# Performance work log

Measured on AMD Instinct MI355X. Metric: run time of the kernel, lower is better.

The kernel has to match this reference:

```python
import jax, jax.numpy as jnp
import numpy as np
import math

N_HEADS = 16
D_EFF = 64
ROPE_BASE = 500.0


def _rope(x, cos, sin):
    # x: (b, h, L, d_eff); cos/sin: (L, d_eff//2)
    x_even = x[..., 0::2]
    x_odd = x[..., 1::2]
    rot = jnp.stack([x_even * cos - x_odd * sin,
                     x_even * sin + x_odd * cos], axis=-1)
    return rot.reshape(x.shape)


def setup_inputs() -> dict:
    key = jax.random.key(0)
    ks = jax.random.split(key, 5)
    B, L, D = 1, 2048, 1024
    X = jax.random.normal(ks[0], (B, L, D), dtype=jnp.float32)
    # causal mask (1 = keep, 0 = masked), broadcastable to (B, h, L, L)
    mask = jnp.tril(jnp.ones((L, L), dtype=jnp.int32))[None, :, :]
    s = 1.0 / math.sqrt(D)
    Wq = jax.random.normal(ks[1], (D, D), dtype=jnp.float32) * s
    Wk = jax.random.normal(ks[2], (D, D), dtype=jnp.float32) * s
    Wv = jax.random.normal(ks[3], (D, D), dtype=jnp.float32) * s
    Wo = jax.random.normal(ks[4], (D, D), dtype=jnp.float32) * s
    return {"X": X, "mask": mask, "Wq": Wq, "Wk": Wk, "Wv": Wv, "Wo": Wo}


def reference(X, mask, Wq, Wk, Wv, Wo):
    b, L, d_model = X.shape
    h, d = N_HEADS, D_EFF
    d_full = h * d

    def split_heads(Y):
        return Y.reshape(b, L, h, d).transpose(0, 2, 1, 3)  # (b,h,L,d)

    Q = split_heads(X @ Wq)
    K = split_heads(X @ Wk)
    V = split_heads(X @ Wv)

    # interleaved RoPE, base 500
    inv_freq = 1.0 / (ROPE_BASE ** (jnp.arange(0, d, 2, dtype=jnp.float32) / d))
    freqs = jnp.arange(L, dtype=jnp.float32)[:, None] * inv_freq  # (L, d/2)
    cos, sin = jnp.cos(freqs), jnp.sin(freqs)
    Q = _rope(Q, cos, sin)
    K = _rope(K, cos, sin)

    S = jnp.einsum('bhqd,bhkd->bhqk', Q, K) / math.sqrt(d)
    S = jnp.where(mask[:, None, :, :] == 0, jnp.float32(-1e9), S)
    # NOTE: faithful to original torch code: softmax over the HEADS axis (dim=1)
    A = jax.nn.softmax(S, axis=1)
    Y = jnp.einsum('bhqk,bhkd->bhqd', A, V)
    Y = Y.transpose(0, 2, 1, 3).reshape(b, L, d_full)
    Y = Y @ Wo
    return Y * math.sqrt(d_model / d_full)
```

## Files before the change

kernel.cpp:

```cpp
#include <hip/hip_runtime.h>
#include <stdint.h>
#include <stddef.h>
#include <math.h>

typedef __attribute__((ext_vector_type(8))) short bf16x8;
typedef __attribute__((ext_vector_type(4))) short short4v;
typedef __attribute__((ext_vector_type(4))) float f32x4;

__device__ __forceinline__ short f2bf(float f) {
  union { float f; uint32_t u; } x; x.f = f;
  return (short)((x.u + 0x7fffu + ((x.u >> 16) & 1u)) >> 16);
}
__device__ __forceinline__ float bf2f(short s) {
  union { uint32_t u; float f; } x; x.u = ((uint32_t)(uint16_t)s) << 16;
  return x.f;
}
__device__ __forceinline__ uint32_t cvt_pk_bf16(float a, float b) {
  uint32_t r;
  asm("v_cvt_pk_bf16_f32 %0, %1, %2" : "=v"(r) : "v"(a), "v"(b));
  return r;
}

__device__ __forceinline__ void gload_lds16(const void* g, void* lds) {
  __builtin_amdgcn_global_load_lds(
      (const __attribute__((address_space(1))) void*)g,
      (__attribute__((address_space(3))) void*)lds, 16, 0, 0);
}

__global__ __launch_bounds__(256) void cast_b(const float* __restrict__ s,
                                              short* __restrict__ d) {
  int i4 = (blockIdx.x * 256 + threadIdx.x) * 4;
  float4 v = *(const float4*)&s[i4];
  short4v r = { f2bf(v.x), f2bf(v.y), f2bf(v.z), f2bf(v.w) };
  *(short4v*)&d[i4] = r;
}

__global__ __launch_bounds__(256) void reduce_y(const short* __restrict__ Ypc,
                                                const float* __restrict__ Cvs,
                                                short* __restrict__ o) {
  int q = blockIdx.x;
  int j = q >> 5, qr = q & 31;
  int a = j >> 2, r = j & 3;
  int base = (a + 1) * (2 * a + r);
  int nch = a + 1;
  int col = threadIdx.x * 4;
  float a0 = Cvs[col + 0], a1 = Cvs[col + 1], a2 = Cvs[col + 2], a3 = Cvs[col + 3];
  const short* p = Ypc + ((size_t)base * 32 + qr) * 1024 + col;
  for (int ch = 0; ch < nch; ch++) {
    short4v v = *(const short4v*)p;
    a0 += bf2f(v[0]); a1 += bf2f(v[1]); a2 += bf2f(v[2]); a3 += bf2f(v[3]);
    p += 32 * 1024;
  }
  uint32_t u0 = cvt_pk_bf16(a0, a1), u1 = cvt_pk_bf16(a2, a3);
  short4v rr = { (short)u0, (short)(u0 >> 16), (short)u1, (short)(u1 >> 16) };
  *(short4v*)&o[(size_t)q * 1024 + col] = rr;
}

__global__ __launch_bounds__(256) void transW(const float* __restrict__ Wq,
                                              const float* __restrict__ Wk,
                                              const float* __restrict__ Wv,
                                              const float* __restrict__ Wo,
                                              short* __restrict__ WcatT,
                                              short* __restrict__ WoT) {
  int z = blockIdx.z;
  const float* src = (z == 0) ? Wq : (z == 1) ? Wk : (z == 2) ? Wv : Wo;
  short* dst = (z == 3) ? WoT : WcatT + (size_t)z * 1024 * 1024;
  __shared__ float tl[32][33];
  int tx = threadIdx.x & 31, ty = threadIdx.x >> 5;
  int kk0 = blockIdx.x * 32;
  int nn0 = blockIdx.y * 32;
#pragma unroll
  for (int j = 0; j < 4; j++)
    tl[ty + j * 8][tx] = src[(size_t)(kk0 + ty + j * 8) * 1024 + nn0 + tx];
  __syncthreads();
#pragma unroll
  for (int j = 0; j < 4; j++)
    dst[(size_t)(nn0 + ty + j * 8) * 1024 + kk0 + tx] = f2bf(tl[tx][ty + j * 8]);
}

__global__ __launch_bounds__(256) void transpose_v(const short* __restrict__ Vb,
                                                   short* __restrict__ Vt) {
  __shared__ short tv[64][72];
  int h = blockIdx.y, k0 = blockIdx.x * 64;
  int tid = threadIdx.x;
#pragma unroll
  for (int j = 0; j < 2; j++) {
    int idx = tid + j * 256;
    int row = idx >> 3, c = idx & 7;
    bf16x8 v = *(const bf16x8*)&Vb[((size_t)h * 2048 + k0 + row) * 64 + c * 8];
#pragma unroll
    for (int t = 0; t < 8; t++) tv[row][c * 8 + t] = v[t];
  }
  __syncthreads();
#pragma unroll
  for (int j = 0; j < 2; j++) {
    int idx = tid + j * 256;
    int d = idx >> 3, c = idx & 7;
    bf16x8 v;
#pragma unroll
    for (int t = 0; t < 8; t++) v[t] = tv[c * 8 + t][d];
    *(bf16x8*)&Vt[((size_t)h * 64 + d) * 2048 + k0 + c * 8] = v;
  }
}

__global__ __launch_bounds__(256) void vsum(const short* __restrict__ Vb,
                                            float* __restrict__ Cvs) {
  __shared__ float red[16][17];
  int h = blockIdx.x >> 2, dq = blockIdx.x & 3;
  int dl = threadIdx.x & 15, ks = threadIdx.x >> 4;
  int d = dq * 16 + dl;
  float acc = 0.f;
  const short* base = &Vb[((size_t)h * 2048 + ks * 128) * 64 + d];
#pragma unroll 8
  for (int k = 0; k < 128; k++) acc += bf2f(base[(size_t)k * 64]);
  red[dl][ks] = acc;
  __syncthreads();
  if (threadIdx.x < 16) {
    float sum = 0.f;
#pragma unroll
    for (int i = 0; i < 16; i++) sum += red[threadIdx.x][i];
    Cvs[h * 64 + dq * 16 + threadIdx.x] = sum * 0.0625f;
  }
}

template <int MODE>
__global__ __launch_bounds__(256, 2)
void gemm_kernel(const short* __restrict__ A, const short* __restrict__ B,
                 int N, int K, float* __restrict__ C,
                 short* __restrict__ Qb, short* __restrict__ Kb,
                 short* __restrict__ Vb) {
  __shared__ __attribute__((aligned(16))) short lga[128 * 64];
  __shared__ __attribute__((aligned(16))) short lgb[128 * 64];
  const int tid = threadIdx.x;
  const int lane = tid & 63;
  const int w = tid >> 6;
  const int l15 = lane & 15;
  const int quad = lane >> 4;
  const int wm = w >> 1, wn = w & 1;
  const int m0 = blockIdx.x * 128, n0 = blockIdx.y * 128;
  const int rsub = lane >> 3;
  const int cpos = lane & 7;

  f32x4 acc[4][4];
#pragma unroll
  for (int i = 0; i < 4; i++)
#pragma unroll
    for (int j = 0; j < 4; j++) acc[i][j] = (f32x4){0.f, 0.f, 0.f, 0.f};

  for (int kb = 0; kb < K; kb += 64) {
    __syncthreads();
#pragma unroll
    for (int j = 0; j < 4; j++) {
      int r = (w * 4 + j) * 8 + rsub;
      int kc = cpos ^ rsub;
      gload_lds16(A + (size_t)(m0 + r) * K + kb + kc * 8, &lga[(w * 4 + j) * 512]);
      gload_lds16(B + (size_t)(n0 + r) * K + kb + kc * 8, &lgb[(w * 4 + j) * 512]);
    }
    __syncthreads();
#pragma unroll
    for (int kk = 0; kk < 2; kk++) {
      bf16x8 af[4], bfr[4];
#pragma unroll
      for (int t = 0; t < 4; t++) {
        int row = wm * 64 + t * 16 + l15;
        int pc = (kk * 4 + quad) ^ (row & 7);
        af[t] = *(const bf16x8*)&lga[row * 64 + pc * 8];
        int rowb = wn * 64 + t * 16 + l15;
        int pcb = (kk * 4 + quad) ^ (rowb & 7);
        bfr[t] = *(const bf16x8*)&lgb[rowb * 64 + pcb * 8];
      }
#pragma unroll
      for (int mt = 0; mt < 4; mt++)
#pragma unroll
        for (int nt = 0; nt < 4; nt++)
          acc[mt][nt] = __builtin_amdgcn_mfma_f32_16x16x32_bf16(
              af[mt], bfr[nt], acc[mt][nt], 0, 0, 0);
    }
  }

  if (MODE == 0) {
#pragma unroll
    for (int mt = 0; mt < 4; mt++) {
      int q = m0 + wm * 64 + mt * 16 + quad * 4;
#pragma unroll
      for (int nt = 0; nt < 4; nt++) {
        int n = n0 + wn * 64 + nt * 16 + l15;
#pragma unroll
        for (int r = 0; r < 4; r++) C[(size_t)(q + r) * N + n] = acc[mt][nt][r];
      }
    }
  } else {
#pragma unroll
    for (int mt = 0; mt < 4; mt++) {
#pragma unroll
      for (int nt = 0; nt < 4; nt++) {
        int n = n0 + wn * 64 + nt * 16 + l15;
        int mat = n >> 10;
        int h = (n >> 6) & 15;
        int d = n & 63;
#pragma unroll
        for (int r = 0; r < 4; r++) {
          int q = m0 + wm * 64 + mt * 16 + quad * 4 + r;
          float v = acc[mt][nt][r];
          float o = __shfl_xor(v, 1, 64);
          if (mat < 2) {
            int i = d >> 1;
            float ang = (float)q * __builtin_exp2f(-(float)i * 0.2801807588956902f);
            float sn, cs;
            __sincosf(ang, &sn, &cs);
            float rv = (d & 1) ? (o * sn + v * cs) : (v * cs - o * sn);
            short* dst = (mat == 0) ? Qb : Kb;
            dst[((size_t)h * 2048 + q) * 64 + d] = f2bf(rv);
          } else {
            Vb[((size_t)h * 2048 + q) * 64 + d] = f2bf(v);
          }
        }
      }
    }
  }
}

__global__ __launch_bounds__(1024, 2)
void attn_kernel(const short* __restrict__ Qb, const short* __restrict__ Kb,
                 const short* __restrict__ Vt, short* __restrict__ Ypc) {
  __shared__ short Sb[16 * 32 * 72];
  const int tid = threadIdx.x;
  const int lane = tid & 63;
  const int h = tid >> 6;
  const int l15 = lane & 15, quad = lane >> 4;
  const int b = blockIdx.x;
  int a = (int)((sqrtf((float)(2 * b + 1)) - 1.f) * 0.5f);
  while (2 * (a + 1) * (a + 2) <= b) a++;
  while (2 * a * (a + 1) > b) a--;
  const int off = b - 2 * a * (a + 1);
  const int den = a + 1;
  const int r = off / den;
  const int c = off - r * den;
  const int j = 4 * a + r;
  const int q0 = j * 32;
  const int G = (j + 2) >> 1;
  const int g0 = 2 * c;
  const int ng = (g0 + 2 <= G) ? 2 : 1;

  bf16x8 qf[2][2];
#pragma unroll
  for (int qs = 0; qs < 2; qs++)
#pragma unroll
    for (int cc = 0; cc < 2; cc++)
      qf[qs][cc] = *(const bf16x8*)&Qb[((size_t)h * 2048 + q0 + qs * 16 + l15) * 64 +
                                       cc * 32 + quad * 8];

  f32x4 yacc[2][4];
#pragma unroll
  for (int i = 0; i < 2; i++)
#pragma unroll
    for (int jj = 0; jj < 4; jj++) yacc[i][jj] = (f32x4){0.f, 0.f, 0.f, 0.f};

  for (int gi = 0; gi < ng; gi++) {
    const int k0 = (g0 + gi) * 64;
#pragma unroll
    for (int st = 0; st < 4; st++) {
      const short* kb = &Kb[((size_t)h * 2048 + k0 + st * 16 + l15) * 64 + quad * 8];
      bf16x8 kf0 = *(const bf16x8*)kb;
      bf16x8 kf1 = *(const bf16x8*)(kb + 32);
#pragma unroll
      for (int qs = 0; qs < 2; qs++) {
        f32x4 sa = (f32x4){0.f, 0.f, 0.f, 0.f};
        sa = __builtin_amdgcn_mfma_f32_16x16x32_bf16(qf[qs][0], kf0, sa, 0, 0, 0);
        sa = __builtin_amdgcn_mfma_f32_16x16x32_bf16(qf[qs][1], kf1, sa, 0, 0, 0);
        const float cs = 0.18033688011112042f;
        uint32_t u0 = cvt_pk_bf16(sa[0] * cs, sa[1] * cs);
        uint32_t u1 = cvt_pk_bf16(sa[2] * cs, sa[3] * cs);
        int rb = (h * 32 + qs * 16 + quad * 4) * 72 + st * 16 + l15;
        Sb[rb]       = (short)u0;
        Sb[rb + 72]  = (short)(u0 >> 16);
        Sb[rb + 144] = (short)u1;
        Sb[rb + 216] = (short)(u1 >> 16);
      }
    }
    __syncthreads();
#pragma unroll
    for (int pp = 0; pp < 2; pp++) {
      int p = tid + pp * 1024;
      int q = p >> 6, kl = p & 63;
      int base = q * 72 + kl;
      float t[16];
      float m = -1e30f;
#pragma unroll
      for (int hh = 0; hh < 16; hh++) {
        t[hh] = bf2f(Sb[hh * 2304 + base]);
        m = fmaxf(m, t[hh]);
      }
      float sum = 0.f;
#pragma unroll
      for (int hh = 0; hh < 16; hh++) {
        float e = __builtin_exp2f(t[hh] - m);
        t[hh] = e;
        sum += e;
      }
      bool msk = (k0 + kl) > (q0 + q);
      float rs = msk ? 0.f : 1.f / sum;
      float offv = msk ? 0.f : 0.0625f;
#pragma unroll
      for (int hh = 0; hh < 16; hh += 2) {
        uint32_t u = cvt_pk_bf16(t[hh] * rs - offv, t[hh + 1] * rs - offv);
        Sb[hh * 2304 + base]       = (short)u;
        Sb[(hh + 1) * 2304 + base] = (short)(u >> 16);
      }
    }
    __syncthreads();
#pragma unroll
    for (int kk = 0; kk < 2; kk++) {
      bf16x8 af0 = *(const bf16x8*)&Sb[(h * 32 + l15) * 72 + kk * 32 + quad * 8];
      bf16x8 af1 = *(const bf16x8*)&Sb[(h * 32 + 16 + l15) * 72 + kk * 32 + quad * 8];
#pragma unroll
      for (int nt = 0; nt < 4; nt++) {
        bf16x8 vf = *(const bf16x8*)&Vt[((size_t)h * 64 + nt * 16 + l15) * 2048 +
                                        k0 + kk * 32 + quad * 8];
        yacc[0][nt] = __builtin_amdgcn_mfma_f32_16x16x32_bf16(af0, vf, yacc[0][nt],
                                                              0, 0, 0);
        yacc[1][nt] = __builtin_amdgcn_mfma_f32_16x16x32_bf16(af1, vf, yacc[1][nt],
                                                              0, 0, 0);
      }
    }
    __syncthreads();
  }
  short* Y = Ypc + (size_t)b * 32 * 1024;
#pragma unroll
  for (int qs = 0; qs < 2; qs++) {
#pragma unroll
    for (int nt = 0; nt < 4; nt++) {
      int col = h * 64 + nt * 16 + l15;
#pragma unroll
      for (int rr = 0; rr < 4; rr++)
        Y[(size_t)(qs * 16 + quad * 4 + rr) * 1024 + col] = f2bf(yacc[qs][nt][rr]);
    }
  }
}

extern "C" void kernel_launch(void* const* d_in, const int* in_sizes, int n_in,
                              void* d_out, int out_size, void* d_ws, size_t ws_size,
                              hipStream_t stream) {
  (void)in_sizes; (void)n_in; (void)out_size; (void)ws_size;
  const float* X  = (const float*)d_in[0];
  const float* Wq = (const float*)d_in[2];
  const float* Wk = (const float*)d_in[3];
  const float* Wv = (const float*)d_in[4];
  const float* Wo = (const float*)d_in[5];
  char* ws = (char*)d_ws;
  const size_t MB = 1024 * 1024;
  short* Xbf   = (short*)(ws + 0);
  short* WcatT = (short*)(ws + 4 * MB);
  short* WoT   = (short*)(ws + 10 * MB);
  short* Qb    = (short*)(ws + 12 * MB);
  short* Kb    = (short*)(ws + 16 * MB);
  short* Vb    = (short*)(ws + 20 * MB);
  short* Vt    = (short*)(ws + 24 * MB);
  short* Ypc   = (short*)(ws + 28 * MB);
  float* Cvs   = (float*)(ws + 63 * MB);
  short* Ycbf  = Xbf;
  float* out   = (float*)d_out;

  cast_b<<<dim3(2048), dim3(256), 0, stream>>>(X, Xbf);
  transW<<<dim3(32, 32, 4), dim3(256), 0, stream>>>(Wq, Wk, Wv, Wo, WcatT, WoT);
  gemm_kernel<1><<<dim3(16, 24), dim3(256), 0, stream>>>(Xbf, WcatT, 3072, 1024,
                                                         nullptr, Qb, Kb, Vb);
  transpose_v<<<dim3(32, 16), dim3(256), 0, stream>>>(Vb, Vt);
  vsum<<<dim3(64), dim3(256), 0, stream>>>(Vb, Cvs);
  attn_kernel<<<dim3(544), dim3(1024), 0, stream>>>(Qb, Kb, Vt, Ypc);
  reduce_y<<<dim3(2048), dim3(256), 0, stream>>>(Ypc, Cvs, Ycbf);
  gemm_kernel<0><<<dim3(16, 8), dim3(256), 0, stream>>>(Ycbf, WoT, 1024, 1024,
                                                        out, nullptr, nullptr, nullptr);
}
```

Before: 223.0 us.

## Double attention query tile to 64 rows with new balanced block-to-chunk mapping

```diff
diff --git a/kernel.cpp b/kernel.cpp
--- a/kernel.cpp
+++ b/kernel.cpp
@@ -39,17 +39,23 @@
                                                 const float* __restrict__ Cvs,
                                                 short* __restrict__ o) {
   int q = blockIdx.x;
-  int j = q >> 5, qr = q & 31;
-  int a = j >> 2, r = j & 3;
-  int base = (a + 1) * (2 * a + r);
-  int nch = a + 1;
+  int j = q >> 6, qr = q & 63;
   int col = threadIdx.x * 4;
   float a0 = Cvs[col + 0], a1 = Cvs[col + 1], a2 = Cvs[col + 2], a3 = Cvs[col + 3];
-  const short* p = Ypc + ((size_t)base * 32 + qr) * 1024 + col;
-  for (int ch = 0; ch < nch; ch++) {
+  int cmax = j >> 1;
+  for (int c = 0; c <= cmax; c++) {
+    int slot;
+    if (j == 2 * c) {
+      slot = 256 + c;
+    } else if (c <= 7) {
+      slot = c + 8 * (j - 2 * c - 1);
+    } else {
+      int x = 15 - c;
+      slot = x + 8 * ((31 - 2 * x) + (j - 2 * c - 1));
+    }
+    const short* p = Ypc + ((size_t)slot * 64 + qr) * 1024 + col;
     short4v v = *(const short4v*)p;
     a0 += bf2f(v[0]); a1 += bf2f(v[1]); a2 += bf2f(v[2]); a3 += bf2f(v[3]);
-    p += 32 * 1024;
   }
   uint32_t u0 = cvt_pk_bf16(a0, a1), u1 = cvt_pk_bf16(a2, a3);
   short4v rr = { (short)u0, (short)(u0 >> 16), (short)u1, (short)(u1 >> 16) };
@@ -220,39 +226,39 @@
   }
 }
 
-__global__ __launch_bounds__(1024, 2)
+__global__ __launch_bounds__(1024, 1)
 void attn_kernel(const short* __restrict__ Qb, const short* __restrict__ Kb,
                  const short* __restrict__ Vt, short* __restrict__ Ypc) {
-  __shared__ short Sb[16 * 32 * 72];
+  __shared__ short Sb[16 * 64 * 72];
   const int tid = threadIdx.x;
   const int lane = tid & 63;
   const int h = tid >> 6;
   const int l15 = lane & 15, quad = lane >> 4;
   const int b = blockIdx.x;
-  int a = (int)((sqrtf((float)(2 * b + 1)) - 1.f) * 0.5f);
-  while (2 * (a + 1) * (a + 2) <= b) a++;
-  while (2 * a * (a + 1) > b) a--;
-  const int off = b - 2 * a * (a + 1);
-  const int den = a + 1;
-  const int r = off / den;
-  const int c = off - r * den;
-  const int j = 4 * a + r;
-  const int q0 = j * 32;
-  const int G = (j + 2) >> 1;
+  int c, j, ng;
+  if (b < 256) {
+    int x = b & 7, s = b >> 3;
+    int n1 = 31 - 2 * x;
+    if (s < n1) { c = x;      j = 2 * x + 1 + s; }
+    else        { c = 15 - x; j = 31 - 2 * x + (s - n1); }
+    ng = 2;
+  } else {
+    c = b - 256; j = 2 * c; ng = 1;
+  }
+  const int q0 = j * 64;
   const int g0 = 2 * c;
-  const int ng = (g0 + 2 <= G) ? 2 : 1;
-
-  bf16x8 qf[2][2];
-#pragma unroll
-  for (int qs = 0; qs < 2; qs++)
+
+  bf16x8 qf[4][2];
+#pragma unroll
+  for (int qs = 0; qs < 4; qs++)
 #pragma unroll
     for (int cc = 0; cc < 2; cc++)
       qf[qs][cc] = *(const bf16x8*)&Qb[((size_t)h * 2048 + q0 + qs * 16 + l15) * 64 +
                                        cc * 32 + quad * 8];
 
-  f32x4 yacc[2][4];
-#pragma unroll
-  for (int i = 0; i < 2; i++)
+  f32x4 yacc[4][4];
+#pragma unroll
+  for (int i = 0; i < 4; i++)
 #pragma unroll
     for (int jj = 0; jj < 4; jj++) yacc[i][jj] = (f32x4){0.f, 0.f, 0.f, 0.f};
 
@@ -264,14 +270,14 @@
       bf16x8 kf0 = *(const bf16x8*)kb;
       bf16x8 kf1 = *(const bf16x8*)(kb + 32);
 #pragma unroll
-      for (int qs = 0; qs < 2; qs++) {
+      for (int qs = 0; qs < 4; qs++) {
         f32x4 sa = (f32x4){0.f, 0.f, 0.f, 0.f};
         sa = __builtin_amdgcn_mfma_f32_16x16x32_bf16(qf[qs][0], kf0, sa, 0, 0, 0);
         sa = __builtin_amdgcn_mfma_f32_16x16x32_bf16(qf[qs][1], kf1, sa, 0, 0, 0);
         const float cs = 0.18033688011112042f;
         uint32_t u0 = cvt_pk_bf16(sa[0] * cs, sa[1] * cs);
         uint32_t u1 = cvt_pk_bf16(sa[2] * cs, sa[3] * cs);
-        int rb = (h * 32 + qs * 16 + quad * 4) * 72 + st * 16 + l15;
+        int rb = (h * 64 + qs * 16 + quad * 4) * 72 + st * 16 + l15;
         Sb[rb]       = (short)u0;
         Sb[rb + 72]  = (short)(u0 >> 16);
         Sb[rb + 144] = (short)u1;
@@ -279,8 +285,8 @@
       }
     }
     __syncthreads();
-#pragma unroll
-    for (int pp = 0; pp < 2; pp++) {
+#pragma unroll 1
+    for (int pp = 0; pp < 4; pp++) {
       int p = tid + pp * 1024;
       int q = p >> 6, kl = p & 63;
       int base = q * 72 + kl;
@@ -288,7 +294,7 @@
       float m = -1e30f;
 #pragma unroll
       for (int hh = 0; hh < 16; hh++) {
-        t[hh] = bf2f(Sb[hh * 2304 + base]);
+        t[hh] = bf2f(Sb[hh * 4608 + base]);
         m = fmaxf(m, t[hh]);
       }
       float sum = 0.f;
@@ -304,30 +310,32 @@
 #pragma unroll
       for (int hh = 0; hh < 16; hh += 2) {
         uint32_t u = cvt_pk_bf16(t[hh] * rs - offv, t[hh + 1] * rs - offv);
-        Sb[hh * 2304 + base]       = (short)u;
-        Sb[(hh + 1) * 2304 + base] = (short)(u >> 16);
+        Sb[hh * 4608 + base]       = (short)u;
+        Sb[(hh + 1) * 4608 + base] = (short)(u >> 16);
       }
     }
     __syncthreads();
 #pragma unroll
     for (int kk = 0; kk < 2; kk++) {
-      bf16x8 af0 = *(const bf16x8*)&Sb[(h * 32 + l15) * 72 + kk * 32 + quad * 8];
-      bf16x8 af1 = *(const bf16x8*)&Sb[(h * 32 + 16 + l15) * 72 + kk * 32 + quad * 8];
+      bf16x8 af[4];
+#pragma unroll
+      for (int qs = 0; qs < 4; qs++)
+        af[qs] = *(const bf16x8*)&Sb[(h * 64 + qs * 16 + l15) * 72 + kk * 32 + quad * 8];
 #pragma unroll
       for (int nt = 0; nt < 4; nt++) {
         bf16x8 vf = *(const bf16x8*)&Vt[((size_t)h * 64 + nt * 16 + l15) * 2048 +
                                         k0 + kk * 32 + quad * 8];
-        yacc[0][nt] = __builtin_amdgcn_mfma_f32_16x16x32_bf16(af0, vf, yacc[0][nt],
-                                                              0, 0, 0);
-        yacc[1][nt] = __builtin_amdgcn_mfma_f32_16x16x32_bf16(af1, vf, yacc[1][nt],
-                                                              0, 0, 0);
-      }
-    }
-    __syncthreads();
-  }
-  short* Y = Ypc + (size_t)b * 32 * 1024;
-#pragma unroll
-  for (int qs = 0; qs < 2; qs++) {
+#pragma unroll
+        for (int qs = 0; qs < 4; qs++)
+          yacc[qs][nt] = __builtin_amdgcn_mfma_f32_16x16x32_bf16(af[qs], vf,
+                                                                 yacc[qs][nt], 0, 0, 0);
+      }
+    }
+    __syncthreads();
+  }
+  short* Y = Ypc + (size_t)b * 64 * 1024;
+#pragma unroll
+  for (int qs = 0; qs < 4; qs++) {
 #pragma unroll
     for (int nt = 0; nt < 4; nt++) {
       int col = h * 64 + nt * 16 + l15;
@@ -367,7 +375,7 @@
                                                          nullptr, Qb, Kb, Vb);
   transpose_v<<<dim3(32, 16), dim3(256), 0, stream>>>(Vb, Vt);
   vsum<<<dim3(64), dim3(256), 0, stream>>>(Vb, Cvs);
-  attn_kernel<<<dim3(544), dim3(1024), 0, stream>>>(Qb, Kb, Vt, Ypc);
+  attn_kernel<<<dim3(272), dim3(1024), 0, stream>>>(Qb, Kb, Vt, Ypc);
   reduce_y<<<dim3(2048), dim3(256), 0, stream>>>(Ypc, Cvs, Ycbf);
   gemm_kernel<0><<<dim3(16, 8), dim3(256), 0, stream>>>(Ycbf, WoT, 1024, 1024,
                                                         out, nullptr, nullptr, nullptr);
```

Result: slower. 232.3 us (+4.2%).

## Remap attention block schedule to balanced slots and drop softmax max pass

Applied to the files above, without the earlier changes.

```diff
diff --git a/kernel.cpp b/kernel.cpp
--- a/kernel.cpp
+++ b/kernel.cpp
@@ -40,16 +40,22 @@
                                                 short* __restrict__ o) {
   int q = blockIdx.x;
   int j = q >> 5, qr = q & 31;
-  int a = j >> 2, r = j & 3;
-  int base = (a + 1) * (2 * a + r);
-  int nch = a + 1;
   int col = threadIdx.x * 4;
   float a0 = Cvs[col + 0], a1 = Cvs[col + 1], a2 = Cvs[col + 2], a3 = Cvs[col + 3];
-  const short* p = Ypc + ((size_t)base * 32 + qr) * 1024 + col;
-  for (int ch = 0; ch < nch; ch++) {
+  int cf = (j - 2) >> 2;
+  for (int c = 0; c <= cf; c++) {
+    int slot = (c <= 7) ? (c + 8 * (j - 4 * c - 2)) : ((15 - c) + 8 * j);
+    const short* p = Ypc + ((size_t)slot * 32 + qr) * 1024 + col;
     short4v v = *(const short4v*)p;
     a0 += bf2f(v[0]); a1 += bf2f(v[1]); a2 += bf2f(v[2]); a3 += bf2f(v[3]);
-    p += 32 * 1024;
+  }
+  if ((j & 3) < 2) {
+    int cp = j >> 2;
+    int slot = (cp <= 7) ? (cp + 8 * (64 + (j & 3)))
+                         : ((15 - cp) + 8 * (66 + (j & 3)));
+    const short* p = Ypc + ((size_t)slot * 32 + qr) * 1024 + col;
+    short4v v = *(const short4v*)p;
+    a0 += bf2f(v[0]); a1 += bf2f(v[1]); a2 += bf2f(v[2]); a3 += bf2f(v[3]);
   }
   uint32_t u0 = cvt_pk_bf16(a0, a1), u1 = cvt_pk_bf16(a2, a3);
   short4v rr = { (short)u0, (short)(u0 >> 16), (short)u1, (short)(u1 >> 16) };
@@ -229,18 +235,15 @@
   const int h = tid >> 6;
   const int l15 = lane & 15, quad = lane >> 4;
   const int b = blockIdx.x;
-  int a = (int)((sqrtf((float)(2 * b + 1)) - 1.f) * 0.5f);
-  while (2 * (a + 1) * (a + 2) <= b) a++;
-  while (2 * a * (a + 1) > b) a--;
-  const int off = b - 2 * a * (a + 1);
-  const int den = a + 1;
-  const int r = off / den;
-  const int c = off - r * den;
-  const int j = 4 * a + r;
+  const int x = b & 7, s = b >> 3;
+  int c, j, ng;
+  const int n1 = 62 - 4 * x;
+  if (s < n1)      { c = x;      j = 4 * x + 2 + s;        ng = 2; }
+  else if (s < 64) { c = 15 - x; j = s;                    ng = 2; }
+  else if (s < 66) { c = x;      j = 4 * x + (s - 64);     ng = 1; }
+  else             { c = 15 - x; j = 60 - 4 * x + (s - 66); ng = 1; }
   const int q0 = j * 32;
-  const int G = (j + 2) >> 1;
   const int g0 = 2 * c;
-  const int ng = (g0 + 2 <= G) ? 2 : 1;
 
   bf16x8 qf[2][2];
 #pragma unroll
@@ -285,16 +288,10 @@
       int q = p >> 6, kl = p & 63;
       int base = q * 72 + kl;
       float t[16];
-      float m = -1e30f;
+      float sum = 0.f;
 #pragma unroll
       for (int hh = 0; hh < 16; hh++) {
-        t[hh] = bf2f(Sb[hh * 2304 + base]);
-        m = fmaxf(m, t[hh]);
-      }
-      float sum = 0.f;
-#pragma unroll
-      for (int hh = 0; hh < 16; hh++) {
-        float e = __builtin_exp2f(t[hh] - m);
+        float e = __builtin_exp2f(bf2f(Sb[hh * 2304 + base]));
         t[hh] = e;
         sum += e;
       }
```

After: 212.3 us. -4.8%, faster.
